# Kernel tuning notes

Measured on AMD Instinct MI355X. Metric: run time of the kernel, lower is better.

## Reference

```python
import jax, jax.numpy as jnp
import numpy as np

N = 20000          # nodes (= masked tokens M, node_ids = arange)
E = 320000         # edges
D_H = 256          # hidden_channels
D_Z = 256          # node_channels
D_A = 256          # attn_channels
D_M = 256          # mlp_hidden_channels
V = 512            # predictor vocab size


def setup_inputs() -> dict:
    key = jax.random.key(0)
    ks = jax.random.split(key, 10)

    def lin(k, fan_in, fan_out):
        return jax.random.normal(k, (fan_in, fan_out), jnp.float32) / np.sqrt(fan_in)

    h_mask = jax.random.normal(ks[0], (N, D_H), jnp.float32)
    z = jax.random.normal(ks[1], (N, D_Z), jnp.float32)
    edge_index = jax.random.randint(ks[2], (2, E), 0, N, dtype=jnp.int32)
    node_ids = jnp.arange(N, dtype=jnp.int32)
    # Pairing of (masked token, edge): with node_ids = arange(N), every edge's
    # dst is a masked node, so masked_idx = dst and edge_idx = arange(E).
    masked_idx = edge_index[1]
    edge_idx = jnp.arange(E, dtype=jnp.int32)
    return {
        "h_mask": h_mask,
        "z": z,
        "Wq": lin(ks[3], D_Z, D_A), "bq": jnp.zeros((D_A,), jnp.float32),
        "Wk": lin(ks[4], D_Z, D_A), "bk": jnp.zeros((D_A,), jnp.float32),
        "W1": lin(ks[5], D_Z, D_M), "b1": jnp.zeros((D_M,), jnp.float32),
        "W2": lin(ks[6], D_M, D_H), "b2": jnp.zeros((D_H,), jnp.float32),
        "Wpred": lin(ks[7], D_H, V), "bpred": jnp.zeros((V,), jnp.float32),
        "edge_index": edge_index,
        "node_ids": node_ids,
        "masked_idx": masked_idx,
        "edge_idx": edge_idx,
    }


def reference(h_mask, z, Wq, bq, Wk, bk, W1, b1, W2, b2, Wpred, bpred,
              edge_index, node_ids, masked_idx, edge_idx):
    src = edge_index[0]
    # Node-level projections (N x D), computed once then gathered per pair.
    q = z @ Wq + bq                      # [N, D_A]
    k = z @ Wk + bk                      # [N, D_A]

    center_nodes = jnp.take(node_ids, masked_idx, axis=0)   # [P]
    neighbor_nodes = jnp.take(src, edge_idx, axis=0)        # [P]

    q_i = jnp.take(q, center_nodes, axis=0)                 # [P, D_A]
    k_j = jnp.take(k, neighbor_nodes, axis=0)               # [P, D_A]
    a_ij = jax.nn.sigmoid(jnp.sum(q_i * k_j, axis=-1, keepdims=True))  # [P, 1]

    h_i = jnp.take(h_mask, masked_idx, axis=0)              # [P, D_H]
    z_j = jnp.take(z, neighbor_nodes, axis=0)               # [P, D_Z]
    g_zj = jax.nn.relu(z_j @ W1 + b1) @ W2 + b2             # [P, D_H]

    h_tilde = a_ij * h_i + (1.0 - a_ij) * g_zj              # [P, D_H]
    edge_logits = h_tilde @ Wpred + bpred                   # [P, V]
    return edge_logits, masked_idx
```

## Files before the change

### kernel.cpp

```cpp
#include <hip/hip_runtime.h>
#include <hip/hip_bf16.h>

typedef __attribute__((ext_vector_type(8))) short s16x8;
typedef __attribute__((ext_vector_type(4))) float f32x4;

__device__ inline float bf2f(unsigned int u16) {
    union { unsigned int i; float f; } v;
    v.i = u16 << 16;
    return v.f;
}
__device__ inline unsigned int f2bf(float f) {
    union { float f; unsigned int i; } v;
    v.f = f;
    return (v.i + 0x7FFFu + ((v.i >> 16) & 1u)) >> 16;
}

__global__ __launch_bounds__(256) void prep_all(
    const float* __restrict__ z, const float* __restrict__ h,
    const float* __restrict__ Wq, const float* __restrict__ Wk,
    const float* __restrict__ W1, const float* __restrict__ W2,
    const float* __restrict__ Wp,
    const float* __restrict__ bq, const float* __restrict__ bk,
    unsigned short* __restrict__ zb, unsigned short* __restrict__ hb,
    unsigned short* __restrict__ Wtqk, unsigned short* __restrict__ Wt1,
    unsigned short* __restrict__ Wt2, unsigned short* __restrict__ Wtp,
    float* __restrict__ bqk, int N)
{
    const int tid = threadIdx.x;
    const int bz = (N * 32 + 255) >> 8;
    int b = blockIdx.x;

    if (b < 2 * bz) {
        const float* src = (b < bz) ? z : h;
        unsigned short* dst = (b < bz) ? zb : hb;
        const int i = (b % bz) * 256 + tid;
        if (i < N * 32) {
            const float4 a = *(const float4*)(src + (size_t)i * 8);
            const float4 c = *(const float4*)(src + (size_t)i * 8 + 4);
            uint4 r;
            r.x = f2bf(a.x) | (f2bf(a.y) << 16);
            r.y = f2bf(a.z) | (f2bf(a.w) << 16);
            r.z = f2bf(c.x) | (f2bf(c.y) << 16);
            r.w = f2bf(c.z) | (f2bf(c.w) << 16);
            *(uint4*)(dst + (size_t)i * 8) = r;
        }
        return;
    }
    b -= 2 * bz;
    if (b < 1024) {
        const int w = b >> 8;
        const int i = (b & 255) * 256 + tid;
        const int k = i >> 8, j = i & 255;
        const float* W = (w == 0) ? Wq : (w == 1) ? Wk : (w == 2) ? W1 : W2;
        unsigned short* Wt = (w == 0) ? Wtqk : (w == 1) ? (Wtqk + 65536)
                              : (w == 2) ? Wt1 : Wt2;
        Wt[j * 256 + k] = (unsigned short)f2bf(W[i]);
        return;
    }
    b -= 1024;
    if (b < 512) {
        const int i = b * 256 + tid;
        const int k = i >> 9, j = i & 511;
        Wtp[(size_t)j * 256 + k] = (unsigned short)f2bf(Wp[i]);
        return;
    }
    b -= 512;
    {
        const int i = b * 256 + tid;
        bqk[i] = (i < 256) ? bq[i] : bk[i - 256];
    }
}

template<bool BIAS, bool RELU>
__global__ __launch_bounds__(256) void gemm_mfma(
    const unsigned short* __restrict__ A0, const unsigned short* __restrict__ A1,
    const unsigned short* __restrict__ Wt, const float* __restrict__ bias,
    unsigned short* __restrict__ out0, unsigned short* __restrict__ out1,
    int M, int Nout)
{
    __shared__ __align__(16) char smem[65536];
    char* ldsA = smem;
    char* ldsB = smem + 32768;
    const unsigned short* A = (blockIdx.y == 0) ? A0 : A1;
    unsigned short* out = (blockIdx.y == 0) ? out0 : out1;

    const int tid  = threadIdx.x;
    const int wid  = tid >> 6, lane = tid & 63;
    const int wr   = wid >> 1, wc = wid & 1;
    const int r0   = blockIdx.x * 64;
    const int swz  = (lane & 7) << 4;

    for (int i = tid; i < 2048; i += 256) {
        const int row = i >> 5, off = i & 31;
        const int gr = r0 + row;
        uint4 v = make_uint4(0, 0, 0, 0);
        if (gr < M) v = *(const uint4*)(A + (size_t)gr * 256 + off * 8);
        const int b = (row * 512 + off * 16) ^ ((row & 7) << 4);
        *(uint4*)(ldsA + b) = v;
    }

    const int ro = lane & 15, ko = (lane >> 4) * 16;
    const int baseA0 = (wr * 32 +  0 + ro) * 512 + ko;
    const int baseA1 = (wr * 32 + 16 + ro) * 512 + ko;
    const int baseB0 = (wc * 32 +  0 + ro) * 512 + ko;
    const int baseB1 = (wc * 32 + 16 + ro) * 512 + ko;

    const int nchunks = Nout >> 6;
    for (int c = 0; c < nchunks; ++c) {
        const int j0 = c << 6;
        for (int i = tid; i < 2048; i += 256) {
            const int row = i >> 5, off = i & 31;
            const uint4 v = *(const uint4*)(Wt + (size_t)(j0 + row) * 256 + off * 8);
            const int b = (row * 512 + off * 16) ^ ((row & 7) << 4);
            *(uint4*)(ldsB + b) = v;
        }
        __syncthreads();

        f32x4 acc00 = {0,0,0,0}, acc01 = {0,0,0,0}, acc10 = {0,0,0,0}, acc11 = {0,0,0,0};
#pragma unroll
        for (int kk = 0; kk < 8; ++kk) {
            const int kb = kk * 64;
            const s16x8 a0 = *(const s16x8*)(ldsA + ((baseA0 + kb) ^ swz));
            const s16x8 a1 = *(const s16x8*)(ldsA + ((baseA1 + kb) ^ swz));
            const s16x8 b0 = *(const s16x8*)(ldsB + ((baseB0 + kb) ^ swz));
            const s16x8 b1 = *(const s16x8*)(ldsB + ((baseB1 + kb) ^ swz));
            acc00 = __builtin_amdgcn_mfma_f32_16x16x32_bf16(a0, b0, acc00, 0, 0, 0);
            acc01 = __builtin_amdgcn_mfma_f32_16x16x32_bf16(a0, b1, acc01, 0, 0, 0);
            acc10 = __builtin_amdgcn_mfma_f32_16x16x32_bf16(a1, b0, acc10, 0, 0, 0);
            acc11 = __builtin_amdgcn_mfma_f32_16x16x32_bf16(a1, b1, acc11, 0, 0, 0);
        }

        const int colb = j0 + wc * 32;
        float bs0 = 0.0f, bs1 = 0.0f;
        if (BIAS) { bs0 = bias[colb + ro]; bs1 = bias[colb + 16 + ro]; }
        const int rb0 = r0 + wr * 32 + (lane >> 4) * 4;
        const int rb1 = rb0 + 16;
#pragma unroll
        for (int r = 0; r < 4; ++r) {
            if (rb0 + r < M) {
                float v0 = acc00[r] + bs0, v1 = acc01[r] + bs1;
                if (RELU) { v0 = fmaxf(v0, 0.0f); v1 = fmaxf(v1, 0.0f); }
                out[(size_t)(rb0 + r) * Nout + colb + ro]      = (unsigned short)f2bf(v0);
                out[(size_t)(rb0 + r) * Nout + colb + 16 + ro] = (unsigned short)f2bf(v1);
            }
            if (rb1 + r < M) {
                float v0 = acc10[r] + bs0, v1 = acc11[r] + bs1;
                if (RELU) { v0 = fmaxf(v0, 0.0f); v1 = fmaxf(v1, 0.0f); }
                out[(size_t)(rb1 + r) * Nout + colb + ro]      = (unsigned short)f2bf(v0);
                out[(size_t)(rb1 + r) * Nout + colb + 16 + ro] = (unsigned short)f2bf(v1);
            }
        }
        __syncthreads();
    }
}

__global__ __launch_bounds__(256) void edge_fused(
    const unsigned short* __restrict__ qkb,
    const unsigned short* __restrict__ hp, const unsigned short* __restrict__ gp,
    const float* __restrict__ bpred,
    const int* __restrict__ edge_src, const int* __restrict__ node_ids,
    const int* __restrict__ masked_idx, const int* __restrict__ edge_idx,
    float* __restrict__ out, int P)
{
    const int wave = threadIdx.x >> 6;
    const int lane = threadIdx.x & 63;
    const int e = blockIdx.x * 4 + wave;
    if (e >= P) return;

    const int mi = masked_idx[e];
    const int c  = node_ids[mi];
    const int s  = edge_src[edge_idx[e]];

    const uint2 qv = *(const uint2*)&qkb[(size_t)c * 512 + lane * 4];
    const uint2 kv = *(const uint2*)&qkb[(size_t)s * 512 + 256 + lane * 4];
    float dot = bf2f(qv.x & 0xFFFFu) * bf2f(kv.x & 0xFFFFu)
              + bf2f(qv.x >> 16)     * bf2f(kv.x >> 16)
              + bf2f(qv.y & 0xFFFFu) * bf2f(kv.y & 0xFFFFu)
              + bf2f(qv.y >> 16)     * bf2f(kv.y >> 16);
#pragma unroll
    for (int off = 32; off; off >>= 1) dot += __shfl_xor(dot, off, 64);

    const float a = 1.0f / (1.0f + expf(-dot));
    const float oma = 1.0f - a;

    const uint4 hv = *(const uint4*)&hp[(size_t)c * 512 + lane * 8];
    const uint4 gv = *(const uint4*)&gp[(size_t)s * 512 + lane * 8];
    const float4 bp0 = *(const float4*)&bpred[lane * 8];
    const float4 bp1 = *(const float4*)&bpred[lane * 8 + 4];

    const unsigned int hw[4] = {hv.x, hv.y, hv.z, hv.w};
    const unsigned int gw[4] = {gv.x, gv.y, gv.z, gv.w};
    const float bp[8] = {bp0.x, bp0.y, bp0.z, bp0.w, bp1.x, bp1.y, bp1.z, bp1.w};

    float res[8];
#pragma unroll
    for (int i = 0; i < 4; ++i) {
        const float h0 = bf2f(hw[i] & 0xFFFFu);
        const float h1 = bf2f(hw[i] >> 16);
        const float g0 = bf2f(gw[i] & 0xFFFFu);
        const float g1 = bf2f(gw[i] >> 16);
        res[2 * i]     = fmaf(a, h0, fmaf(oma, g0, bp[2 * i]));
        res[2 * i + 1] = fmaf(a, h1, fmaf(oma, g1, bp[2 * i + 1]));
    }
    float* dst = &out[(size_t)e * 512 + lane * 8];
    *(float4*)(dst)     = make_float4(res[0], res[1], res[2], res[3]);
    *(float4*)(dst + 4) = make_float4(res[4], res[5], res[6], res[7]);

    if (lane == 0) {
        out[(size_t)P * 512 + e] = (float)mi;
    }
}

extern "C" void kernel_launch(void* const* d_in, const int* in_sizes, int n_in,
                              void* d_out, int out_size, void* d_ws, size_t ws_size,
                              hipStream_t stream) {
    const float* h_mask = (const float*)d_in[0];
    const float* z      = (const float*)d_in[1];
    const float* Wq     = (const float*)d_in[2];
    const float* bq     = (const float*)d_in[3];
    const float* Wk     = (const float*)d_in[4];
    const float* bk     = (const float*)d_in[5];
    const float* W1     = (const float*)d_in[6];
    const float* b1     = (const float*)d_in[7];
    const float* W2     = (const float*)d_in[8];
    const float* b2     = (const float*)d_in[9];
    const float* Wpred  = (const float*)d_in[10];
    const float* bpred  = (const float*)d_in[11];
    const int* edge_index = (const int*)d_in[12];
    const int* node_ids   = (const int*)d_in[13];
    const int* masked_idx = (const int*)d_in[14];
    const int* edge_idx   = (const int*)d_in[15];

    const int N = in_sizes[13];
    const int P = in_sizes[14];

    unsigned short* zb   = (unsigned short*)d_ws;
    unsigned short* hb   = zb   + (size_t)N * 256;
    unsigned short* qkb  = hb   + (size_t)N * 256;
    unsigned short* tb   = qkb  + (size_t)N * 512;
    unsigned short* gb   = tb   + (size_t)N * 256;
    unsigned short* gpb  = gb   + (size_t)N * 256;
    unsigned short* hpb  = gpb  + (size_t)N * 512;
    unsigned short* Wtqk = hpb  + (size_t)N * 512;
    unsigned short* Wt1  = Wtqk + 131072;
    unsigned short* Wt2  = Wt1  + 65536;
    unsigned short* Wtp  = Wt2  + 65536;
    float*          bqk  = (float*)(Wtp + 131072);

    const dim3 blk(256);
    const int bz   = (N * 32 + 255) / 256;
    const int gb64 = (N + 63) / 64;
    const int eb   = (P + 3) / 4;

    prep_all<<<dim3(2 * bz + 1024 + 512 + 2), blk, 0, stream>>>(
        z, h_mask, Wq, Wk, W1, W2, Wpred, bq, bk,
        zb, hb, Wtqk, Wt1, Wt2, Wtp, bqk, N);

    gemm_mfma<true, false><<<dim3(gb64, 1), blk, 0, stream>>>(zb, nullptr, Wtqk, bqk, qkb, nullptr, N, 512);
    gemm_mfma<true, true ><<<dim3(gb64, 1), blk, 0, stream>>>(zb, nullptr, Wt1, b1, tb, nullptr, N, 256);
    gemm_mfma<true, false><<<dim3(gb64, 1), blk, 0, stream>>>(tb, nullptr, Wt2, b2, gb, nullptr, N, 256);
    gemm_mfma<false, false><<<dim3(gb64, 2), blk, 0, stream>>>(hb, gb, Wtp, nullptr, hpb, gpb, N, 512);

    edge_fused<<<dim3(eb), blk, 0, stream>>>(qkb, hpb, gpb, bpred,
                                             edge_index, node_ids, masked_idx, edge_idx,
                                             (float*)d_out, P);
}
```

Before: 364.8 us.

## Fuse fp32-to-bf16 input conversion into GEMMs and merge QK/W1 and h-pred launches

Input conversion of z and h_mask to bf16 moves out of the prep kernel and into the GEMM A-tile load, so the bf16 copies of the activations are never written. The Q, K and W1 projections are merged into one 768-wide GEMM job with a column-split store and ReLU applied only to the W1 range. The h_mask·Wpred job runs in the same launch as that merged job via a two-job grid, which raises parallelism. The price is a generic per-element store path with runtime bias, ReLU-range and split branches, plus more launches for the g path (three GEMM launches instead of four overall, but serialized differently).

```diff
diff --git a/kernel.cpp b/kernel.cpp
--- a/kernel.cpp
+++ b/kernel.cpp
@@ -15,46 +15,24 @@
     return (v.i + 0x7FFFu + ((v.i >> 16) & 1u)) >> 16;
 }
 
-__global__ __launch_bounds__(256) void prep_all(
-    const float* __restrict__ z, const float* __restrict__ h,
+__global__ __launch_bounds__(256) void prep_w(
     const float* __restrict__ Wq, const float* __restrict__ Wk,
     const float* __restrict__ W1, const float* __restrict__ W2,
     const float* __restrict__ Wp,
     const float* __restrict__ bq, const float* __restrict__ bk,
-    unsigned short* __restrict__ zb, unsigned short* __restrict__ hb,
-    unsigned short* __restrict__ Wtqk, unsigned short* __restrict__ Wt1,
-    unsigned short* __restrict__ Wt2, unsigned short* __restrict__ Wtp,
-    float* __restrict__ bqk, int N)
+    const float* __restrict__ b1,
+    unsigned short* __restrict__ Wtqkt, unsigned short* __restrict__ Wt2,
+    unsigned short* __restrict__ Wtp, float* __restrict__ bqkt)
 {
     const int tid = threadIdx.x;
-    const int bz = (N * 32 + 255) >> 8;
     int b = blockIdx.x;
-
-    if (b < 2 * bz) {
-        const float* src = (b < bz) ? z : h;
-        unsigned short* dst = (b < bz) ? zb : hb;
-        const int i = (b % bz) * 256 + tid;
-        if (i < N * 32) {
-            const float4 a = *(const float4*)(src + (size_t)i * 8);
-            const float4 c = *(const float4*)(src + (size_t)i * 8 + 4);
-            uint4 r;
-            r.x = f2bf(a.x) | (f2bf(a.y) << 16);
-            r.y = f2bf(a.z) | (f2bf(a.w) << 16);
-            r.z = f2bf(c.x) | (f2bf(c.y) << 16);
-            r.w = f2bf(c.z) | (f2bf(c.w) << 16);
-            *(uint4*)(dst + (size_t)i * 8) = r;
-        }
-        return;
-    }
-    b -= 2 * bz;
     if (b < 1024) {
         const int w = b >> 8;
         const int i = (b & 255) * 256 + tid;
         const int k = i >> 8, j = i & 255;
         const float* W = (w == 0) ? Wq : (w == 1) ? Wk : (w == 2) ? W1 : W2;
-        unsigned short* Wt = (w == 0) ? Wtqk : (w == 1) ? (Wtqk + 65536)
-                              : (w == 2) ? Wt1 : Wt2;
-        Wt[j * 256 + k] = (unsigned short)f2bf(W[i]);
+        unsigned short* dst = (w == 3) ? Wt2 : (Wtqkt + w * 65536);
+        dst[j * 256 + k] = (unsigned short)f2bf(W[i]);
         return;
     }
     b -= 1024;
@@ -67,22 +45,37 @@
     b -= 512;
     {
         const int i = b * 256 + tid;
-        bqk[i] = (i < 256) ? bq[i] : bk[i - 256];
-    }
-}
-
-template<bool BIAS, bool RELU>
-__global__ __launch_bounds__(256) void gemm_mfma(
-    const unsigned short* __restrict__ A0, const unsigned short* __restrict__ A1,
-    const unsigned short* __restrict__ Wt, const float* __restrict__ bias,
-    unsigned short* __restrict__ out0, unsigned short* __restrict__ out1,
-    int M, int Nout)
+        bqkt[i] = (i < 256) ? bq[i] : (i < 512) ? bk[i - 256] : b1[i - 512];
+    }
+}
+
+struct GemmJob {
+    const void* A;
+    const unsigned short* Wt;
+    const float* bias;
+    unsigned short* out1;
+    unsigned short* out2;
+    int Nout;
+    int split;
+    int relu_lo, relu_hi;
+    int a_f32;
+};
+
+__device__ inline void job_store(const GemmJob& J, int row, int col, float v, int M) {
+    if (row >= M) return;
+    if (J.bias) v += J.bias[col];
+    if (col >= J.relu_lo && col < J.relu_hi) v = fmaxf(v, 0.0f);
+    if (col < J.split) J.out1[(size_t)row * J.split + col] = (unsigned short)f2bf(v);
+    else J.out2[(size_t)row * (J.Nout - J.split) + (col - J.split)] = (unsigned short)f2bf(v);
+}
+
+__global__ __launch_bounds__(256) void gemm_multi(
+    GemmJob j0, GemmJob j1, int M)
 {
     __shared__ __align__(16) char smem[65536];
     char* ldsA = smem;
     char* ldsB = smem + 32768;
-    const unsigned short* A = (blockIdx.y == 0) ? A0 : A1;
-    unsigned short* out = (blockIdx.y == 0) ? out0 : out1;
+    const GemmJob J = (blockIdx.y == 0) ? j0 : j1;
 
     const int tid  = threadIdx.x;
     const int wid  = tid >> 6, lane = tid & 63;
@@ -90,13 +83,33 @@
     const int r0   = blockIdx.x * 64;
     const int swz  = (lane & 7) << 4;
 
-    for (int i = tid; i < 2048; i += 256) {
-        const int row = i >> 5, off = i & 31;
-        const int gr = r0 + row;
-        uint4 v = make_uint4(0, 0, 0, 0);
-        if (gr < M) v = *(const uint4*)(A + (size_t)gr * 256 + off * 8);
-        const int b = (row * 512 + off * 16) ^ ((row & 7) << 4);
-        *(uint4*)(ldsA + b) = v;
+    if (J.a_f32) {
+        const float* Af = (const float*)J.A;
+        for (int i = tid; i < 2048; i += 256) {
+            const int row = i >> 5, off = i & 31;
+            const int gr = r0 + row;
+            uint4 v = make_uint4(0, 0, 0, 0);
+            if (gr < M) {
+                const float4 a = *(const float4*)(Af + (size_t)gr * 256 + off * 8);
+                const float4 c = *(const float4*)(Af + (size_t)gr * 256 + off * 8 + 4);
+                v.x = f2bf(a.x) | (f2bf(a.y) << 16);
+                v.y = f2bf(a.z) | (f2bf(a.w) << 16);
+                v.z = f2bf(c.x) | (f2bf(c.y) << 16);
+                v.w = f2bf(c.z) | (f2bf(c.w) << 16);
+            }
+            const int b = (row * 512 + off * 16) ^ ((row & 7) << 4);
+            *(uint4*)(ldsA + b) = v;
+        }
+    } else {
+        const unsigned short* Ab = (const unsigned short*)J.A;
+        for (int i = tid; i < 2048; i += 256) {
+            const int row = i >> 5, off = i & 31;
+            const int gr = r0 + row;
+            uint4 v = make_uint4(0, 0, 0, 0);
+            if (gr < M) v = *(const uint4*)(Ab + (size_t)gr * 256 + off * 8);
+            const int b = (row * 512 + off * 16) ^ ((row & 7) << 4);
+            *(uint4*)(ldsA + b) = v;
+        }
     }
 
     const int ro = lane & 15, ko = (lane >> 4) * 16;
@@ -105,12 +118,12 @@
     const int baseB0 = (wc * 32 +  0 + ro) * 512 + ko;
     const int baseB1 = (wc * 32 + 16 + ro) * 512 + ko;
 
-    const int nchunks = Nout >> 6;
+    const int nchunks = J.Nout >> 6;
     for (int c = 0; c < nchunks; ++c) {
-        const int j0 = c << 6;
+        const int j0c = c << 6;
         for (int i = tid; i < 2048; i += 256) {
             const int row = i >> 5, off = i & 31;
-            const uint4 v = *(const uint4*)(Wt + (size_t)(j0 + row) * 256 + off * 8);
+            const uint4 v = *(const uint4*)(J.Wt + (size_t)(j0c + row) * 256 + off * 8);
             const int b = (row * 512 + off * 16) ^ ((row & 7) << 4);
             *(uint4*)(ldsB + b) = v;
         }
@@ -130,25 +143,15 @@
             acc11 = __builtin_amdgcn_mfma_f32_16x16x32_bf16(a1, b1, acc11, 0, 0, 0);
         }
 
-        const int colb = j0 + wc * 32;
-        float bs0 = 0.0f, bs1 = 0.0f;
-        if (BIAS) { bs0 = bias[colb + ro]; bs1 = bias[colb + 16 + ro]; }
+        const int colb = j0c + wc * 32;
         const int rb0 = r0 + wr * 32 + (lane >> 4) * 4;
         const int rb1 = rb0 + 16;
 #pragma unroll
         for (int r = 0; r < 4; ++r) {
-            if (rb0 + r < M) {
-                float v0 = acc00[r] + bs0, v1 = acc01[r] + bs1;
-                if (RELU) { v0 = fmaxf(v0, 0.0f); v1 = fmaxf(v1, 0.0f); }
-                out[(size_t)(rb0 + r) * Nout + colb + ro]      = (unsigned short)f2bf(v0);
-                out[(size_t)(rb0 + r) * Nout + colb + 16 + ro] = (unsigned short)f2bf(v1);
-            }
-            if (rb1 + r < M) {
-                float v0 = acc10[r] + bs0, v1 = acc11[r] + bs1;
-                if (RELU) { v0 = fmaxf(v0, 0.0f); v1 = fmaxf(v1, 0.0f); }
-                out[(size_t)(rb1 + r) * Nout + colb + ro]      = (unsigned short)f2bf(v0);
-                out[(size_t)(rb1 + r) * Nout + colb + 16 + ro] = (unsigned short)f2bf(v1);
-            }
+            job_store(J, rb0 + r, colb + ro,      acc00[r], M);
+            job_store(J, rb0 + r, colb + 16 + ro, acc01[r], M);
+            job_store(J, rb1 + r, colb + ro,      acc10[r], M);
+            job_store(J, rb1 + r, colb + 16 + ro, acc11[r], M);
         }
         __syncthreads();
     }
@@ -234,32 +237,32 @@
     const int N = in_sizes[13];
     const int P = in_sizes[14];
 
-    unsigned short* zb   = (unsigned short*)d_ws;
-    unsigned short* hb   = zb   + (size_t)N * 256;
-    unsigned short* qkb  = hb   + (size_t)N * 256;
-    unsigned short* tb   = qkb  + (size_t)N * 512;
-    unsigned short* gb   = tb   + (size_t)N * 256;
-    unsigned short* gpb  = gb   + (size_t)N * 256;
-    unsigned short* hpb  = gpb  + (size_t)N * 512;
-    unsigned short* Wtqk = hpb  + (size_t)N * 512;
-    unsigned short* Wt1  = Wtqk + 131072;
-    unsigned short* Wt2  = Wt1  + 65536;
-    unsigned short* Wtp  = Wt2  + 65536;
-    float*          bqk  = (float*)(Wtp + 131072);
+    unsigned short* qkb   = (unsigned short*)d_ws;
+    unsigned short* tb    = qkb   + (size_t)N * 512;
+    unsigned short* gb    = tb    + (size_t)N * 256;
+    unsigned short* gpb   = gb    + (size_t)N * 256;
+    unsigned short* hpb   = gpb   + (size_t)N * 512;
+    unsigned short* Wtqkt = hpb   + (size_t)N * 512;
+    unsigned short* Wt2   = Wtqkt + 196608;
+    unsigned short* Wtp   = Wt2   + 65536;
+    float*          bqkt  = (float*)(Wtp + 131072);
 
     const dim3 blk(256);
-    const int bz   = (N * 32 + 255) / 256;
     const int gb64 = (N + 63) / 64;
     const int eb   = (P + 3) / 4;
 
-    prep_all<<<dim3(2 * bz + 1024 + 512 + 2), blk, 0, stream>>>(
-        z, h_mask, Wq, Wk, W1, W2, Wpred, bq, bk,
-        zb, hb, Wtqk, Wt1, Wt2, Wtp, bqk, N);
-
-    gemm_mfma<true, false><<<dim3(gb64, 1), blk, 0, stream>>>(zb, nullptr, Wtqk, bqk, qkb, nullptr, N, 512);
-    gemm_mfma<true, true ><<<dim3(gb64, 1), blk, 0, stream>>>(zb, nullptr, Wt1, b1, tb, nullptr, N, 256);
-    gemm_mfma<true, false><<<dim3(gb64, 1), blk, 0, stream>>>(tb, nullptr, Wt2, b2, gb, nullptr, N, 256);
-    gemm_mfma<false, false><<<dim3(gb64, 2), blk, 0, stream>>>(hb, gb, Wtp, nullptr, hpb, gpb, N, 512);
+    prep_w<<<dim3(1024 + 512 + 3), blk, 0, stream>>>(
+        Wq, Wk, W1, W2, Wpred, bq, bk, b1, Wtqkt, Wt2, Wtp, bqkt);
+
+    GemmJob a0 = { z,      Wtqkt, bqkt,    qkb, tb,      768, 512, 512, 768, 1 };
+    GemmJob a1 = { h_mask, Wtp,   nullptr, hpb, nullptr, 512, 512, 0,   0,   1 };
+    gemm_multi<<<dim3(gb64, 2), blk, 0, stream>>>(a0, a1, N);
+
+    GemmJob b0 = { tb, Wt2, b2, gb, nullptr, 256, 256, 0, 0, 0 };
+    gemm_multi<<<dim3(gb64, 1), blk, 0, stream>>>(b0, b0, N);
+
+    GemmJob c0 = { gb, Wtp, nullptr, gpb, nullptr, 512, 512, 0, 0, 0 };
+    gemm_multi<<<dim3(gb64, 1), blk, 0, stream>>>(c0, c0, N);
 
     edge_fused<<<dim3(eb), blk, 0, stream>>>(qkb, hpb, gpb, bpred,
                                              edge_index, node_ids, masked_idx, edge_idx,
```

Measured after the change: 366.7 us. About the same (+0.5%).
